# Performance work log

Hardware: AMD Instinct MI355X
Metric: run time of the kernel (lower is better)

## Reference

```python
import jax, jax.numpy as jnp
import numpy as np

B, I, C, K, L = 4, 4, 256, 7, 5
SIZES = [160, 80, 40, 20, 10]


def setup_inputs() -> dict:
    key = jax.random.key(0)
    ks = jax.random.split(key, 10)
    inp = {}
    for i, s in enumerate(SIZES):
        inp[f"feats_x{i}"] = jax.random.normal(ks[i], (B, C, s, s), jnp.float32)
    inp["modulator"] = jax.random.normal(ks[5], (B, I, C, K, K), jnp.float32)
    # conv weights ~ normal_init(std=0.01), biases zero
    inp["pm_w"] = 0.01 * jax.random.normal(ks[6], (L, C, C, K, K), jnp.float32)
    inp["pm_b"] = jnp.zeros((L, C), jnp.float32)
    inp["po_w"] = 0.01 * jax.random.normal(ks[7], (L, C, C), jnp.float32)
    inp["po_b"] = jnp.zeros((L, C), jnp.float32)
    return inp


def reference(feats_x0, feats_x1, feats_x2, feats_x3, feats_x4,
              modulator, pm_w, pm_b, po_w, po_b):
    """Batched version of RPN_Modulator.inference: for every (image i, instance j,
    level k): q = Conv7x7(modulator[i,j]) -> [C,1,1]; out = Conv1x1(q * feats_x[k][i]).
    Vectorized over images and instances instead of nested Python loops."""
    feats = [feats_x0, feats_x1, feats_x2, feats_x3, feats_x4]
    outs = []
    for k in range(L):
        # 7x7 valid conv on a 7x7 crop == full contraction -> per-instance channel vector
        q = jnp.einsum('bichw,ochw->bio', modulator, pm_w[k]) + pm_b[k]  # [B,I,C]
        # channel-wise modulation of the gallery feature map
        m = q[:, :, :, None, None] * feats[k][:, None]                   # [B,I,C,H,W]
        # 1x1 output projection
        o = jnp.einsum('bichw,oc->biohw', m, po_w[k]) \
            + po_b[k][None, None, :, None, None]                          # [B,I,C,H,W]
        outs.append(o)
    return tuple(outs)
```

## Files before the change

### kernel.cpp

```cpp
#include <hip/hip_runtime.h>
#include <hip/hip_bf16.h>


typedef __bf16 bf16x8 __attribute__((ext_vector_type(8)));
typedef float  f32x4  __attribute__((ext_vector_type(4)));
typedef unsigned short u16;

__device__ __forceinline__ unsigned pack2(float lo, float hi) {
    __hip_bfloat162 h = __float22bfloat162_rn(make_float2(lo, hi));
    union { __hip_bfloat162 h; unsigned u; } cv; cv.h = h; return cv.u;
}

__device__ __forceinline__ void decode_tile(int x, int& k, int& nt, int& N, size_t& oo) {
    if (x < 200)      { k = 0; nt = x;       N = 25600; oo = 0; }
    else if (x < 250) { k = 1; nt = x - 200; N = 6400;  oo = 104857600; }
    else if (x < 263) { k = 2; nt = x - 250; N = 1600;  oo = 131072000; }
    else if (x < 267) { k = 3; nt = x - 263; N = 400;   oo = 137625600; }
    else              { k = 4; nt = x - 267; N = 100;   oo = 139264000; }
}

__global__ __launch_bounds__(256) void k_q(
    const float* __restrict__ modulator,
    const float* __restrict__ pm_w,
    float* __restrict__ qpart)
{
    int o4 = blockIdx.x;
    int k  = blockIdx.y;
    int s  = blockIdx.z;
    int t  = threadIdx.x;
    float acc[4][16];
#pragma unroll
    for (int j = 0; j < 4; ++j)
#pragma unroll
        for (int bi = 0; bi < 16; ++bi) acc[j][bi] = 0.f;
    const float4* mod4 = (const float4*)modulator;
    const float4* wp0 = (const float4*)(pm_w + ((size_t)k * 256 + o4      ) * 12544);
    const float4* wp1 = (const float4*)(pm_w + ((size_t)k * 256 + o4 +  64) * 12544);
    const float4* wp2 = (const float4*)(pm_w + ((size_t)k * 256 + o4 + 128) * 12544);
    const float4* wp3 = (const float4*)(pm_w + ((size_t)k * 256 + o4 + 192) * 12544);
    for (int it = 0; it < 4; ++it) {
        int jj = it * 256 + t;
        if (jj < 784) {
            int jx = s * 784 + jj;
            float4 wv0 = wp0[jx], wv1 = wp1[jx], wv2 = wp2[jx], wv3 = wp3[jx];
#pragma unroll
            for (int bi = 0; bi < 16; ++bi) {
                float4 m = mod4[bi * 3136 + jx];
                acc[0][bi] += wv0.x * m.x + wv0.y * m.y + wv0.z * m.z + wv0.w * m.w;
                acc[1][bi] += wv1.x * m.x + wv1.y * m.y + wv1.z * m.z + wv1.w * m.w;
                acc[2][bi] += wv2.x * m.x + wv2.y * m.y + wv2.z * m.z + wv2.w * m.w;
                acc[3][bi] += wv3.x * m.x + wv3.y * m.y + wv3.z * m.z + wv3.w * m.w;
            }
        }
    }
#pragma unroll
    for (int j = 0; j < 4; ++j)
#pragma unroll
        for (int bi = 0; bi < 16; ++bi)
#pragma unroll
            for (int off = 32; off > 0; off >>= 1)
                acc[j][bi] += __shfl_down(acc[j][bi], off);
    __shared__ float red[4][64];
    int w = t >> 6, lane = t & 63;
    if (lane == 0) {
#pragma unroll
        for (int j = 0; j < 4; ++j)
#pragma unroll
            for (int bi = 0; bi < 16; ++bi) red[w][j * 16 + bi] = acc[j][bi];
    }
    __syncthreads();
    if (t < 64) {
        float v = red[0][t] + red[1][t] + red[2][t] + red[3][t];
        int bi = t & 15;
        int o  = o4 + (t >> 4) * 64;
        qpart[(((size_t)s * 5 + k) * 16 + bi) * 256 + o] = v;
    }
}

__global__ __launch_bounds__(256) void k_w2(
    const float* __restrict__ po_w,
    const float* __restrict__ pm_b,
    const float* __restrict__ qpart,
    u16* __restrict__ w2)
{
    int idx4 = blockIdx.x * 256 + threadIdx.x;
    int c4 = idx4 & 63;
    int o  = (idx4 >> 6) & 255;
    int bi = (idx4 >> 14) & 15;
    int k  = idx4 >> 18;
    size_t qi = ((size_t)(k * 16 + bi)) * 256 + c4 * 4;
    f32x4 q0 = *(const f32x4*)(qpart + qi);
    f32x4 q1 = *(const f32x4*)(qpart + qi + 20480);
    f32x4 q2 = *(const f32x4*)(qpart + qi + 40960);
    f32x4 q3 = *(const f32x4*)(qpart + qi + 61440);
    f32x4 pb = *(const f32x4*)(pm_b + k * 256 + c4 * 4);
    f32x4 q  = q0 + q1 + q2 + q3 + pb;
    f32x4 w  = *(const f32x4*)(po_w + ((size_t)(k * 256 + o)) * 256 + c4 * 4);
    uint2 r;
    r.x = pack2(w[0] * q[0], w[1] * q[1]);
    r.y = pack2(w[2] * q[2], w[3] * q[3]);
    *(uint2*)(w2 + (size_t)idx4 * 4) = r;
}

__global__ __launch_bounds__(512, 4) void k_gemm(
    const float* __restrict__ f0, const float* __restrict__ f1,
    const float* __restrict__ f2, const float* __restrict__ f3,
    const float* __restrict__ f4,
    const u16* __restrict__ w2,
    const float* __restrict__ po_b,
    float* __restrict__ out)
{
    __shared__ __align__(16) u16 ldsB[128 * 256];
    int k, nt, N; size_t oo;
    decode_tile(blockIdx.x, k, nt, N, oo);
    const float* fsrc = (k == 0) ? f0 : (k == 1) ? f1 : (k == 2) ? f2 : (k == 3) ? f3 : f4;
    const int b = blockIdx.y;
    const int t = threadIdx.x;
    const int n0 = nt * 128;

    {
        const float* s = fsrc + (size_t)b * 256 * N + n0;
        int ng = t & 31, grp = t >> 5;
        bool inb = (n0 + ng * 4) < N;
#pragma unroll
        for (int j = 0; j < 8; ++j) {
            int p = j * 16 + grp;
            f32x4 v0 = {0.f, 0.f, 0.f, 0.f}, v1 = {0.f, 0.f, 0.f, 0.f};
            if (inb) {
                v0 = *(const f32x4*)(s + (size_t)(2 * p) * N + ng * 4);
                v1 = *(const f32x4*)(s + (size_t)(2 * p + 1) * N + ng * 4);
            }
#pragma unroll
            for (int e = 0; e < 4; ++e) {
                int n = ng * 4 + e;
                unsigned off = (unsigned)(n << 9) + (unsigned)(p << 2);
                off ^= (unsigned)((n & 7) << 4);
                *(unsigned*)((char*)ldsB + off) = pack2(v0[e], v1[e]);
            }
        }
    }
    __syncthreads();

    const int lane = t & 63, w = t >> 6;
    const int lr = lane & 15, lg = lane >> 4;
    const float* pb = po_b + k * 256;
    float* obase0 = out + oo;

#pragma unroll 1
    for (int i = 0; i < 4; ++i) {
        const u16* wsrc = w2 + ((size_t)(k * 16 + b * 4 + i) << 16);
        float* obase = obase0 + (size_t)(b * 4 + i) * 256 * N;
        f32x4 acc[2][8];
#pragma unroll
        for (int mi = 0; mi < 2; ++mi)
#pragma unroll
            for (int ni = 0; ni < 8; ++ni)
                acc[mi][ni] = (f32x4){0.f, 0.f, 0.f, 0.f};

#pragma unroll 2
        for (int kk = 0; kk < 8; ++kk) {
            bf16x8 a[2], bb[8];
#pragma unroll
            for (int mi = 0; mi < 2; ++mi)
                a[mi] = *(const bf16x8*)(wsrc + (size_t)(w * 32 + mi * 16 + lr) * 256 + kk * 32 + lg * 8);
#pragma unroll
            for (int ni = 0; ni < 8; ++ni) {
                int row = ni * 16 + lr;
                unsigned off = (unsigned)(row << 9) + (unsigned)(kk << 6) + (unsigned)(lg << 4);
                off ^= (unsigned)((row & 7) << 4);
                bb[ni] = *(const bf16x8*)((const char*)ldsB + off);
            }
#pragma unroll
            for (int mi = 0; mi < 2; ++mi)
#pragma unroll
                for (int ni = 0; ni < 8; ++ni)
                    acc[mi][ni] = __builtin_amdgcn_mfma_f32_16x16x32_bf16(a[mi], bb[ni], acc[mi][ni], 0, 0, 0);
        }

#pragma unroll
        for (int mi = 0; mi < 2; ++mi) {
#pragma unroll
            for (int rr = 0; rr < 4; ++rr) {
                int orow = w * 32 + mi * 16 + lg * 4 + rr;
                float bias = pb[orow];
#pragma unroll
                for (int ni = 0; ni < 8; ++ni) {
                    int ocol = n0 + ni * 16 + lr;
                    if (ocol < N)
                        __builtin_nontemporal_store(acc[mi][ni][rr] + bias,
                                                    obase + (size_t)orow * N + ocol);
                }
            }
        }
    }
}

extern "C" void kernel_launch(void* const* d_in, const int* in_sizes, int n_in,
                              void* d_out, int out_size, void* d_ws, size_t ws_size,
                              hipStream_t stream) {
    const float* f0 = (const float*)d_in[0];
    const float* f1 = (const float*)d_in[1];
    const float* f2 = (const float*)d_in[2];
    const float* f3 = (const float*)d_in[3];
    const float* f4 = (const float*)d_in[4];
    const float* modulator = (const float*)d_in[5];
    const float* pm_w = (const float*)d_in[6];
    const float* pm_b = (const float*)d_in[7];
    const float* po_w = (const float*)d_in[8];
    const float* po_b = (const float*)d_in[9];
    float* out = (float*)d_out;

    u16* w2 = (u16*)d_ws;
    float* qpart = (float*)(w2 + (size_t)5 * 16 * 256 * 256);

    k_q<<<dim3(64, 5, 4), 256, 0, stream>>>(modulator, pm_w, qpart);
    k_w2<<<5120, 256, 0, stream>>>(po_w, pm_b, qpart, w2);
    k_gemm<<<dim3(268, 4), 512, 0, stream>>>(f0, f1, f2, f3, f4, w2, po_b, out);
}
```

Baseline: 223.2 us.

## Switch GEMM to 32x32x16 MFMA with new LDS swizzle and bias-initialized accumulators

Replaces the 16x16x32 bf16 MFMA tiling (2x8 tiles per wave) with 32x32x16 MFMA (4 tiles per wave). This reduces the A-operand loads and the LDS reads per K step. The LDS staging now packs four channels per 8-byte store and uses a new XOR swizzle that matches the new read pattern. Bias is preloaded once and used to initialise the accumulators, which removes the per-row bias loads in the epilogue. The cost is a different output store pattern and changed register pressure.

```diff
diff --git a/kernel.cpp b/kernel.cpp
--- a/kernel.cpp
+++ b/kernel.cpp
@@ -4,6 +4,7 @@
 
 typedef __bf16 bf16x8 __attribute__((ext_vector_type(8)));
 typedef float  f32x4  __attribute__((ext_vector_type(4)));
+typedef float  f32x16 __attribute__((ext_vector_type(16)));
 typedef unsigned short u16;
 
 __device__ __forceinline__ unsigned pack2(float lo, float hi) {
@@ -119,76 +120,87 @@
     const int n0 = nt * 128;
 
     {
-        const float* s = fsrc + (size_t)b * 256 * N + n0;
-        int ng = t & 31, grp = t >> 5;
-        bool inb = (n0 + ng * 4) < N;
-#pragma unroll
-        for (int j = 0; j < 8; ++j) {
-            int p = j * 16 + grp;
-            f32x4 v0 = {0.f, 0.f, 0.f, 0.f}, v1 = {0.f, 0.f, 0.f, 0.f};
+        const int ng = t & 31, grp = t >> 5;
+        const bool inb = (n0 + ng * 4) < N;
+        const float* s = fsrc + (size_t)b * 256 * N + n0 + ng * 4;
+#pragma unroll
+        for (int j = 0; j < 4; ++j) {
+            int q = j * 16 + grp;
+            f32x4 v0 = {0.f,0.f,0.f,0.f}, v1 = {0.f,0.f,0.f,0.f};
+            f32x4 v2 = {0.f,0.f,0.f,0.f}, v3 = {0.f,0.f,0.f,0.f};
             if (inb) {
-                v0 = *(const f32x4*)(s + (size_t)(2 * p) * N + ng * 4);
-                v1 = *(const f32x4*)(s + (size_t)(2 * p + 1) * N + ng * 4);
+                v0 = *(const f32x4*)(s + (size_t)(4 * q + 0) * N);
+                v1 = *(const f32x4*)(s + (size_t)(4 * q + 1) * N);
+                v2 = *(const f32x4*)(s + (size_t)(4 * q + 2) * N);
+                v3 = *(const f32x4*)(s + (size_t)(4 * q + 3) * N);
             }
 #pragma unroll
             for (int e = 0; e < 4; ++e) {
                 int n = ng * 4 + e;
-                unsigned off = (unsigned)(n << 9) + (unsigned)(p << 2);
-                off ^= (unsigned)((n & 7) << 4);
-                *(unsigned*)((char*)ldsB + off) = pack2(v0[e], v1[e]);
+                unsigned h = ((unsigned)n & 7u) ^ (((unsigned)n >> 2) & 7u);
+                unsigned off = ((unsigned)n << 9) + ((unsigned)q << 3);
+                off ^= (h << 4);
+                uint2 wv; wv.x = pack2(v0[e], v1[e]); wv.y = pack2(v2[e], v3[e]);
+                *(uint2*)((char*)ldsB + off) = wv;
             }
         }
     }
     __syncthreads();
 
     const int lane = t & 63, w = t >> 6;
-    const int lr = lane & 15, lg = lane >> 4;
+    const int l31 = lane & 31, lg5 = lane >> 5;
     const float* pb = po_b + k * 256;
     float* obase0 = out + oo;
 
+    f32x4 bias4[4];
+#pragma unroll
+    for (int m = 0; m < 4; ++m)
+        bias4[m] = *(const f32x4*)(pb + w * 32 + 8 * m + 4 * lg5);
+
+    unsigned mrow[4], mx[4];
+#pragma unroll
+    for (int ni = 0; ni < 4; ++ni) {
+        int row = ni * 32 + l31;
+        unsigned h = ((unsigned)row & 7u) ^ (((unsigned)row >> 2) & 7u);
+        mrow[ni] = (unsigned)row << 9;
+        mx[ni] = ((unsigned)lg5 ^ h) << 4;
+    }
+
 #pragma unroll 1
     for (int i = 0; i < 4; ++i) {
-        const u16* wsrc = w2 + ((size_t)(k * 16 + b * 4 + i) << 16);
+        const u16* wsrc = w2 + ((size_t)(k * 16 + b * 4 + i) << 16)
+                        + (size_t)(w * 32 + l31) * 256 + lg5 * 8;
         float* obase = obase0 + (size_t)(b * 4 + i) * 256 * N;
-        f32x4 acc[2][8];
-#pragma unroll
-        for (int mi = 0; mi < 2; ++mi)
-#pragma unroll
-            for (int ni = 0; ni < 8; ++ni)
-                acc[mi][ni] = (f32x4){0.f, 0.f, 0.f, 0.f};
+
+        f32x16 acc[4];
+#pragma unroll
+        for (int ni = 0; ni < 4; ++ni)
+#pragma unroll
+            for (int q = 0; q < 16; ++q)
+                acc[ni][q] = bias4[q >> 2][q & 3];
 
 #pragma unroll 2
-        for (int kk = 0; kk < 8; ++kk) {
-            bf16x8 a[2], bb[8];
-#pragma unroll
-            for (int mi = 0; mi < 2; ++mi)
-                a[mi] = *(const bf16x8*)(wsrc + (size_t)(w * 32 + mi * 16 + lr) * 256 + kk * 32 + lg * 8);
-#pragma unroll
-            for (int ni = 0; ni < 8; ++ni) {
-                int row = ni * 16 + lr;
-                unsigned off = (unsigned)(row << 9) + (unsigned)(kk << 6) + (unsigned)(lg << 4);
-                off ^= (unsigned)((row & 7) << 4);
-                bb[ni] = *(const bf16x8*)((const char*)ldsB + off);
-            }
-#pragma unroll
-            for (int mi = 0; mi < 2; ++mi)
-#pragma unroll
-                for (int ni = 0; ni < 8; ++ni)
-                    acc[mi][ni] = __builtin_amdgcn_mfma_f32_16x16x32_bf16(a[mi], bb[ni], acc[mi][ni], 0, 0, 0);
-        }
-
-#pragma unroll
-        for (int mi = 0; mi < 2; ++mi) {
-#pragma unroll
-            for (int rr = 0; rr < 4; ++rr) {
-                int orow = w * 32 + mi * 16 + lg * 4 + rr;
-                float bias = pb[orow];
-#pragma unroll
-                for (int ni = 0; ni < 8; ++ni) {
-                    int ocol = n0 + ni * 16 + lr;
-                    if (ocol < N)
-                        __builtin_nontemporal_store(acc[mi][ni][rr] + bias,
-                                                    obase + (size_t)orow * N + ocol);
+        for (int kk = 0; kk < 16; ++kk) {
+            bf16x8 a = *(const bf16x8*)(wsrc + kk * 16);
+            bf16x8 bb[4];
+            unsigned kb = (unsigned)kk << 5;
+#pragma unroll
+            for (int ni = 0; ni < 4; ++ni)
+                bb[ni] = *(const bf16x8*)((const char*)ldsB + (mrow[ni] + (kb ^ mx[ni])));
+#pragma unroll
+            for (int ni = 0; ni < 4; ++ni)
+                acc[ni] = __builtin_amdgcn_mfma_f32_32x32x16_bf16(a, bb[ni], acc[ni], 0, 0, 0);
+        }
+
+#pragma unroll
+        for (int ni = 0; ni < 4; ++ni) {
+            int ocol = n0 + ni * 32 + l31;
+            if (ocol < N) {
+                float* op = obase + ocol;
+#pragma unroll
+                for (int q = 0; q < 16; ++q) {
+                    int orow = w * 32 + (q & 3) + 8 * (q >> 2) + 4 * lg5;
+                    __builtin_nontemporal_store(acc[ni][q], op + (size_t)orow * N);
                 }
             }
         }
```

Result: faster. 193.5 us, median of 2 (-13.3%).
